# Optimization experiments

Hardware: AMD Instinct MI355X
Metric: run time of the kernel (lower is better)

Reference implementation:

```python
import jax, jax.numpy as jnp
import numpy as np

N_NODES = 1048576
N_EDGES = 4 * N_NODES

def _mlp(h, w1, b1, w2, b2):
    return jax.nn.relu(h @ w1 + b1) @ w2 + b2

def setup_inputs() -> dict:
    key = jax.random.key(0)
    ks = jax.random.split(key, 12)
    def glorot(k, shape):
        fan_in, fan_out = shape
        lim = np.sqrt(6.0 / (fan_in + fan_out)).astype(np.float32)
        return jax.random.uniform(k, shape, jnp.float32, -lim, lim)
    x = jax.random.normal(ks[0], (N_NODES, 3), jnp.float32)
    edge_index = jax.random.randint(ks[1], (2, N_EDGES), 0, N_NODES, jnp.int64 if jax.config.jax_enable_x64 else jnp.int32)
    edge_attr = jax.random.normal(ks[2], (N_EDGES, 1), jnp.float32)
    u = jax.random.normal(ks[3], (1, 3), jnp.float32)
    batch = jnp.zeros((N_NODES,), jnp.int32)
    return {
        'x': x, 'edge_index': edge_index, 'edge_attr': edge_attr, 'u': u, 'batch': batch,
        'w1a': glorot(ks[4], (4, 20)), 'b1a': jnp.zeros((20,), jnp.float32),
        'w1b': glorot(ks[5], (20, 3)), 'b1b': jnp.zeros((3,), jnp.float32),
        'w2a': glorot(ks[6], (6, 20)), 'b2a': jnp.zeros((20,), jnp.float32),
        'w2b': glorot(ks[7], (20, 3)), 'b2b': jnp.zeros((3,), jnp.float32),
    }

def reference(x, edge_index, edge_attr, u, batch, w1a, b1a, w1b, b1b, w2a, b2a, w2b, b2b):
    row, col = edge_index[0], edge_index[1]
    n = x.shape[0]
    # gather source node feats, concat edge attr -> [E,4]
    h = jnp.concatenate([x[row], edge_attr], axis=1)
    h = _mlp(h, w1a, b1a, w1b, b1b)                    # [E,3]
    # scatter-mean over destination nodes
    s = jax.ops.segment_sum(h, col, num_segments=n)    # [N,3]
    cnt = jax.ops.segment_sum(jnp.ones((h.shape[0],), h.dtype), col, num_segments=n)
    agg = s / jnp.maximum(cnt, 1.0)[:, None]
    out = _mlp(jnp.concatenate([x, agg], axis=1), w2a, b2a, w2b, b2b)  # [N,3]
    fac = jnp.sqrt(jnp.sum(out ** 2, axis=1, keepdims=True))
    return out / fac
```

## Files before the change

kernel.cpp:

```cpp
#include <hip/hip_runtime.h>


#define SEG  4096
#define P1T  256
#define P1I  (SEG / P1T)
#define BKSH 12
#define BKN  4096
#define NBK  256
#define PFXW 257
#define P2T  1024
#define P2W  (P2T / 64)

union HCvt { _Float16 h; unsigned short u; };

__device__ __forceinline__ float h2f(unsigned short u) {
    HCvt c; c.u = u; return (float)c.h;
}

__device__ __forceinline__ unsigned long long mlp1_pack(
    float in0, float in1, float in2, float in3,
    const float* sw1a, const float* sb1a, const float* sw1b, const float* sb1b)
{
    float h1[20];
#pragma unroll
    for (int j = 0; j < 20; ++j) {
        float v = sb1a[j];
        v = fmaf(in0, sw1a[0 * 20 + j], v);
        v = fmaf(in1, sw1a[1 * 20 + j], v);
        v = fmaf(in2, sw1a[2 * 20 + j], v);
        v = fmaf(in3, sw1a[3 * 20 + j], v);
        h1[j] = v > 0.f ? v : 0.f;
    }
    float o0 = sb1b[0], o1 = sb1b[1], o2 = sb1b[2];
#pragma unroll
    for (int j = 0; j < 20; ++j) {
        o0 = fmaf(h1[j], sw1b[j * 3 + 0], o0);
        o1 = fmaf(h1[j], sw1b[j * 3 + 1], o1);
        o2 = fmaf(h1[j], sw1b[j * 3 + 2], o2);
    }
    o0 = fminf(fmaxf(o0, -8.0f), 8.0f - 2.0f / 2048.0f);
    o1 = fminf(fmaxf(o1, -8.0f), 8.0f - 2.0f / 2048.0f);
    o2 = fminf(fmaxf(o2, -8.0f), 8.0f - 2.0f / 1024.0f);
    const unsigned int q0 = (unsigned int)__float2int_rn((o0 + 8.0f) * 2048.0f);
    const unsigned int q1 = (unsigned int)__float2int_rn((o1 + 8.0f) * 2048.0f);
    const unsigned int q2 = (unsigned int)__float2int_rn((o2 + 8.0f) * 1024.0f);
    return 1ULL | ((unsigned long long)q0 << 5)
                | ((unsigned long long)q1 << 25)
                | ((unsigned long long)q2 << 45);
}

__global__ __launch_bounds__(256) void pack_x_kernel(
    const float* __restrict__ x, ushort4* __restrict__ xp, int N)
{
    const int n = blockIdx.x * 256 + threadIdx.x;
    if (n >= N) return;
    HCvt c0, c1, c2;
    c0.h = (_Float16)x[n * 3 + 0];
    c1.h = (_Float16)x[n * 3 + 1];
    c2.h = (_Float16)x[n * 3 + 2];
    ushort4 r; r.x = c0.u; r.y = c1.u; r.z = c2.u; r.w = 0;
    xp[n] = r;
}

__global__ __launch_bounds__(P1T) void p1_kernel(
    const ushort4* __restrict__ xp,
    const int*   __restrict__ edge_index,
    const float* __restrict__ edge_attr,
    const float* __restrict__ w1a, const float* __restrict__ b1a,
    const float* __restrict__ w1b, const float* __restrict__ b1b,
    unsigned short* __restrict__ pfx_t,
    unsigned short* __restrict__ cols16,
    unsigned long long* __restrict__ vals,
    int E)
{
    __shared__ float sw1a[80], sb1a[20], sw1b[60], sb1b[3];
    __shared__ unsigned int hist[NBK];
    __shared__ unsigned int sc[NBK];
    __shared__ unsigned int pfx[PFXW];
    __shared__ unsigned short scols[SEG];
    __shared__ __align__(16) unsigned long long svals[SEG];
    const int t = threadIdx.x;
    if (t < 80) sw1a[t] = w1a[t];
    if (t < 20) sb1a[t] = b1a[t];
    if (t < 60) sw1b[t] = w1b[t];
    if (t < 3)  sb1b[t] = b1b[t];
    hist[t] = 0;
    __syncthreads();

    const int s = blockIdx.x;
    const int base = s * SEG;

    unsigned int col8[P1I];
#pragma unroll
    for (int i = 0; i < P1I; ++i) {
        const int e = base + i * P1T + t;
        if (e < E) {
            const unsigned int c = (unsigned int)edge_index[E + e];
            col8[i] = c;
            atomicAdd(&hist[c >> BKSH], 1u);
        } else {
            col8[i] = 0xFFFFFFFFu;
        }
    }
    __syncthreads();

    sc[t] = hist[t];
    __syncthreads();
#pragma unroll
    for (int off = 1; off < NBK; off <<= 1) {
        const unsigned int u = (t >= off) ? sc[t - off] : 0u;
        __syncthreads();
        sc[t] += u;
        __syncthreads();
    }
    pfx[t + 1] = sc[t];
    if (t == 0) pfx[0] = 0;
    hist[t] = 0;
    __syncthreads();

    pfx_t[s * PFXW + t] = (unsigned short)pfx[t];
    if (t == 0) pfx_t[s * PFXW + NBK] = (unsigned short)pfx[NBK];

#pragma unroll
    for (int i = 0; i < P1I; ++i) {
        const unsigned int c = col8[i];
        if (c == 0xFFFFFFFFu) continue;
        const int e = base + i * P1T + t;
        const int row = edge_index[e];
        const float in3 = edge_attr[e];
        const ushort4 px = xp[row];
        const float in0 = h2f(px.x);
        const float in1 = h2f(px.y);
        const float in2 = h2f(px.z);
        const unsigned long long val =
            mlp1_pack(in0, in1, in2, in3, sw1a, sb1a, sw1b, sb1b);
        const unsigned int bkt = c >> BKSH;
        const unsigned int r = atomicAdd(&hist[bkt], 1u);
        const unsigned int idx = pfx[bkt] + r;
        scols[idx] = (unsigned short)(c & (BKN - 1));
        svals[idx] = val;
    }
    __syncthreads();

    unsigned int* gc = (unsigned int*)(cols16 + (size_t)base);
    const unsigned int* scu = (const unsigned int*)scols;
#pragma unroll
    for (int k = t; k < SEG / 2; k += P1T) gc[k] = scu[k];
    unsigned long long* gv = vals + (size_t)base;
#pragma unroll
    for (int k = t; k < SEG; k += P1T) gv[k] = svals[k];
}

__global__ __launch_bounds__(P2T) void p2_kernel(
    const float* __restrict__ x,
    const unsigned short* __restrict__ pfx_t,
    const unsigned short* __restrict__ cols16,
    const unsigned long long* __restrict__ vals,
    const float* __restrict__ w2a, const float* __restrict__ b2a,
    const float* __restrict__ w2b, const float* __restrict__ b2b,
    float* __restrict__ out,
    int N, int nsegs)
{
    __shared__ float sw2a[120], sb2a[20], sw2b[60], sb2b[3];
    __shared__ unsigned long long acc[BKN];
    const int t = threadIdx.x;
    if (t < 120) sw2a[t] = w2a[t];
    if (t < 20)  sb2a[t] = b2a[t];
    if (t < 60)  sw2b[t] = w2b[t];
    if (t < 3)   sb2b[t] = b2b[t];
#pragma unroll
    for (int k = 0; k < BKN / P2T; ++k) acc[k * P2T + t] = 0ULL;
    __syncthreads();

    const int b = blockIdx.x;
    const int wave = t >> 6;
    const int lane = t & 63;

    for (int s = wave; s < nsegs; s += P2W) {
        const unsigned int pa = pfx_t[s * PFXW + b];
        const unsigned int pb = pfx_t[s * PFXW + b + 1];
        const size_t base = (size_t)s * SEG;
        for (unsigned int i = pa + lane; i < pb; i += 64) {
            const unsigned int c = cols16[base + i];
            const unsigned long long v = vals[base + i];
            atomicAdd(&acc[c], v);
        }
    }
    __syncthreads();

    const int node0 = b * BKN;
#pragma unroll
    for (int k = 0; k < BKN / P2T; ++k) {
        const int n = node0 + k * P2T + t;
        if (n >= N) continue;
        const unsigned long long q = acc[k * P2T + t];

        const float cnt = (float)(unsigned int)(q & 31ULL);
        const float f0 = (float)(unsigned int)((q >> 5)  & 0xFFFFFULL);
        const float f1 = (float)(unsigned int)((q >> 25) & 0xFFFFFULL);
        const float f2 = (float)(unsigned int)(q >> 45);
        const float s0 = f0 * (1.0f / 2048.0f) - 8.0f * cnt;
        const float s1 = f1 * (1.0f / 2048.0f) - 8.0f * cnt;
        const float s2 = f2 * (1.0f / 1024.0f) - 8.0f * cnt;
        const float invc = 1.0f / fmaxf(cnt, 1.0f);

        const float in0 = x[n * 3 + 0];
        const float in1 = x[n * 3 + 1];
        const float in2 = x[n * 3 + 2];
        const float in3 = s0 * invc;
        const float in4 = s1 * invc;
        const float in5 = s2 * invc;

        float h1[20];
#pragma unroll
        for (int j = 0; j < 20; ++j) {
            float v = sb2a[j];
            v = fmaf(in0, sw2a[0 * 20 + j], v);
            v = fmaf(in1, sw2a[1 * 20 + j], v);
            v = fmaf(in2, sw2a[2 * 20 + j], v);
            v = fmaf(in3, sw2a[3 * 20 + j], v);
            v = fmaf(in4, sw2a[4 * 20 + j], v);
            v = fmaf(in5, sw2a[5 * 20 + j], v);
            h1[j] = v > 0.f ? v : 0.f;
        }
        float o0 = sb2b[0], o1 = sb2b[1], o2 = sb2b[2];
#pragma unroll
        for (int j = 0; j < 20; ++j) {
            o0 = fmaf(h1[j], sw2b[j * 3 + 0], o0);
            o1 = fmaf(h1[j], sw2b[j * 3 + 1], o1);
            o2 = fmaf(h1[j], sw2b[j * 3 + 2], o2);
        }
        const float inv = 1.0f / sqrtf(o0 * o0 + o1 * o1 + o2 * o2);
        out[n * 3 + 0] = o0 * inv;
        out[n * 3 + 1] = o1 * inv;
        out[n * 3 + 2] = o2 * inv;
    }
}

__global__ __launch_bounds__(256) void edge_kernel_fb(
    const float* __restrict__ x, const int* __restrict__ edge_index,
    const float* __restrict__ edge_attr,
    const float* __restrict__ w1a, const float* __restrict__ b1a,
    const float* __restrict__ w1b, const float* __restrict__ b1b,
    unsigned long long* __restrict__ acc, int E)
{
    __shared__ float sw1a[80], sb1a[20], sw1b[60], sb1b[3];
    const int t = threadIdx.x;
    if (t < 80) sw1a[t] = w1a[t];
    if (t < 20) sb1a[t] = b1a[t];
    if (t < 60) sw1b[t] = w1b[t];
    if (t < 3)  sb1b[t] = b1b[t];
    __syncthreads();
    const int e = blockIdx.x * 256 + t;
    if (e >= E) return;
    const int row = edge_index[e];
    const int col = edge_index[E + e];
    const unsigned long long val = mlp1_pack(
        x[row * 3 + 0], x[row * 3 + 1], x[row * 3 + 2], edge_attr[e],
        sw1a, sb1a, sw1b, sb1b);
    atomicAdd(acc + col, val);
}

__global__ __launch_bounds__(256) void node_kernel_fb(
    const float* __restrict__ x, const unsigned long long* __restrict__ acc,
    const float* __restrict__ w2a, const float* __restrict__ b2a,
    const float* __restrict__ w2b, const float* __restrict__ b2b,
    float* __restrict__ out, int N)
{
    __shared__ float sw2a[120], sb2a[20], sw2b[60], sb2b[3];
    const int t = threadIdx.x;
    if (t < 120) sw2a[t] = w2a[t];
    if (t < 20)  sb2a[t] = b2a[t];
    if (t < 60)  sw2b[t] = w2b[t];
    if (t < 3)   sb2b[t] = b2b[t];
    __syncthreads();
    const int n = blockIdx.x * 256 + t;
    if (n >= N) return;
    const unsigned long long q = acc[n];
    const float cnt = (float)(unsigned int)(q & 31ULL);
    const float f0 = (float)(unsigned int)((q >> 5)  & 0xFFFFFULL);
    const float f1 = (float)(unsigned int)((q >> 25) & 0xFFFFFULL);
    const float f2 = (float)(unsigned int)(q >> 45);
    const float s0 = f0 * (1.0f / 2048.0f) - 8.0f * cnt;
    const float s1 = f1 * (1.0f / 2048.0f) - 8.0f * cnt;
    const float s2 = f2 * (1.0f / 1024.0f) - 8.0f * cnt;
    const float invc = 1.0f / fmaxf(cnt, 1.0f);
    const float in0 = x[n * 3 + 0], in1 = x[n * 3 + 1], in2 = x[n * 3 + 2];
    const float in3 = s0 * invc, in4 = s1 * invc, in5 = s2 * invc;
    float h1[20];
#pragma unroll
    for (int j = 0; j < 20; ++j) {
        float v = sb2a[j];
        v = fmaf(in0, sw2a[0 * 20 + j], v);
        v = fmaf(in1, sw2a[1 * 20 + j], v);
        v = fmaf(in2, sw2a[2 * 20 + j], v);
        v = fmaf(in3, sw2a[3 * 20 + j], v);
        v = fmaf(in4, sw2a[4 * 20 + j], v);
        v = fmaf(in5, sw2a[5 * 20 + j], v);
        h1[j] = v > 0.f ? v : 0.f;
    }
    float o0 = sb2b[0], o1 = sb2b[1], o2 = sb2b[2];
#pragma unroll
    for (int j = 0; j < 20; ++j) {
        o0 = fmaf(h1[j], sw2b[j * 3 + 0], o0);
        o1 = fmaf(h1[j], sw2b[j * 3 + 1], o1);
        o2 = fmaf(h1[j], sw2b[j * 3 + 2], o2);
    }
    const float inv = 1.0f / sqrtf(o0 * o0 + o1 * o1 + o2 * o2);
    out[n * 3 + 0] = o0 * inv;
    out[n * 3 + 1] = o1 * inv;
    out[n * 3 + 2] = o2 * inv;
}

extern "C" void kernel_launch(void* const* d_in, const int* in_sizes, int n_in,
                              void* d_out, int out_size, void* d_ws, size_t ws_size,
                              hipStream_t stream) {
    const float* x          = (const float*)d_in[0];
    const int*   edge_index = (const int*)  d_in[1];
    const float* edge_attr  = (const float*)d_in[2];
    const float* w1a = (const float*)d_in[5];
    const float* b1a = (const float*)d_in[6];
    const float* w1b = (const float*)d_in[7];
    const float* b1b = (const float*)d_in[8];
    const float* w2a = (const float*)d_in[9];
    const float* b2a = (const float*)d_in[10];
    const float* w2b = (const float*)d_in[11];
    const float* b2b = (const float*)d_in[12];

    const int N = in_sizes[0] / 3;
    const int E = in_sizes[2];

    const int nbuckets = (N + BKN - 1) / BKN;
    const int nsegs = (E + SEG - 1) / SEG;

    const size_t xp_bytes   = (size_t)N * sizeof(ushort4);
    const size_t pfx_off    = (xp_bytes + 255) & ~(size_t)255;
    const size_t pfx_bytes  = (size_t)nsegs * PFXW * sizeof(unsigned short);
    const size_t cols_off   = (pfx_off + pfx_bytes + 255) & ~(size_t)255;
    const size_t cols_bytes = (size_t)nsegs * SEG * sizeof(unsigned short);
    const size_t vals_off   = (cols_off + cols_bytes + 255) & ~(size_t)255;
    const size_t need       = vals_off + (size_t)nsegs * SEG * sizeof(unsigned long long);

    const bool fast = (nbuckets <= NBK) && (ws_size >= need);

    if (fast) {
        ushort4* xp = (ushort4*)d_ws;
        unsigned short* pfx_t  = (unsigned short*)((char*)d_ws + pfx_off);
        unsigned short* cols16 = (unsigned short*)((char*)d_ws + cols_off);
        unsigned long long* vals = (unsigned long long*)((char*)d_ws + vals_off);

        pack_x_kernel<<<(N + 255) / 256, 256, 0, stream>>>(x, xp, N);

        p1_kernel<<<nsegs, P1T, 0, stream>>>(
            xp, edge_index, edge_attr, w1a, b1a, w1b, b1b,
            pfx_t, cols16, vals, E);

        p2_kernel<<<nbuckets, P2T, 0, stream>>>(
            x, pfx_t, cols16, vals, w2a, b2a, w2b, b2b,
            (float*)d_out, N, nsegs);
    } else {
        unsigned long long* acc = (unsigned long long*)d_ws;
        hipMemsetAsync(acc, 0, (size_t)N * sizeof(unsigned long long), stream);
        edge_kernel_fb<<<(E + 255) / 256, 256, 0, stream>>>(
            x, edge_index, edge_attr, w1a, b1a, w1b, b1b, acc, E);
        node_kernel_fb<<<(N + 255) / 256, 256, 0, stream>>>(
            x, acc, w2a, b2a, w2b, b2b, (float*)d_out, N);
    }
}
```

Measured before the change: 238.9 us.

## Split bucket aggregation into two half-blocks and separate node MLP kernel

The per-bucket scatter-add phase now runs as two blocks per bucket, each covering half of the segments and writing a partial accumulator to global memory. A new elementwise kernel sums the two partials and runs the node MLP and normalisation. The prefix table is stored transposed so each bucket reads a contiguous row, and the edge kernel block grows to 512 threads. The goal is more blocks in flight than 256 buckets give, at the cost of an extra launch and a round trip of the partial sums through global memory.

Measured after the change: 283.4 us. 18.6% more time.

```diff
diff --git a/kernel.cpp b/kernel.cpp
--- a/kernel.cpp
+++ b/kernel.cpp
@@ -2,14 +2,13 @@
 
 
 #define SEG  4096
-#define P1T  256
+#define P1T  512
 #define P1I  (SEG / P1T)
 #define BKSH 12
 #define BKN  4096
 #define NBK  256
 #define PFXW 257
-#define P2T  1024
-#define P2W  (P2T / 64)
+#define P2AT 512
 
 union HCvt { _Float16 h; unsigned short u; };
 
@@ -49,6 +48,51 @@
                 | ((unsigned long long)q2 << 45);
 }
 
+__device__ __forceinline__ void mlp2_store(
+    unsigned long long q, const float* __restrict__ x, float* __restrict__ out,
+    int n, const float* sw2a, const float* sb2a, const float* sw2b, const float* sb2b)
+{
+    const float cnt = (float)(unsigned int)(q & 31ULL);
+    const float f0 = (float)(unsigned int)((q >> 5)  & 0xFFFFFULL);
+    const float f1 = (float)(unsigned int)((q >> 25) & 0xFFFFFULL);
+    const float f2 = (float)(unsigned int)(q >> 45);
+    const float s0 = f0 * (1.0f / 2048.0f) - 8.0f * cnt;
+    const float s1 = f1 * (1.0f / 2048.0f) - 8.0f * cnt;
+    const float s2 = f2 * (1.0f / 1024.0f) - 8.0f * cnt;
+    const float invc = 1.0f / fmaxf(cnt, 1.0f);
+
+    const float in0 = x[n * 3 + 0];
+    const float in1 = x[n * 3 + 1];
+    const float in2 = x[n * 3 + 2];
+    const float in3 = s0 * invc;
+    const float in4 = s1 * invc;
+    const float in5 = s2 * invc;
+
+    float h1[20];
+#pragma unroll
+    for (int j = 0; j < 20; ++j) {
+        float v = sb2a[j];
+        v = fmaf(in0, sw2a[0 * 20 + j], v);
+        v = fmaf(in1, sw2a[1 * 20 + j], v);
+        v = fmaf(in2, sw2a[2 * 20 + j], v);
+        v = fmaf(in3, sw2a[3 * 20 + j], v);
+        v = fmaf(in4, sw2a[4 * 20 + j], v);
+        v = fmaf(in5, sw2a[5 * 20 + j], v);
+        h1[j] = v > 0.f ? v : 0.f;
+    }
+    float o0 = sb2b[0], o1 = sb2b[1], o2 = sb2b[2];
+#pragma unroll
+    for (int j = 0; j < 20; ++j) {
+        o0 = fmaf(h1[j], sw2b[j * 3 + 0], o0);
+        o1 = fmaf(h1[j], sw2b[j * 3 + 1], o1);
+        o2 = fmaf(h1[j], sw2b[j * 3 + 2], o2);
+    }
+    const float inv = 1.0f / sqrtf(o0 * o0 + o1 * o1 + o2 * o2);
+    out[n * 3 + 0] = o0 * inv;
+    out[n * 3 + 1] = o1 * inv;
+    out[n * 3 + 2] = o2 * inv;
+}
+
 __global__ __launch_bounds__(256) void pack_x_kernel(
     const float* __restrict__ x, ushort4* __restrict__ xp, int N)
 {
@@ -62,16 +106,16 @@
     xp[n] = r;
 }
 
-__global__ __launch_bounds__(P1T) void p1_kernel(
+__global__ __launch_bounds__(P1T, 4) void p1_kernel(
     const ushort4* __restrict__ xp,
     const int*   __restrict__ edge_index,
     const float* __restrict__ edge_attr,
     const float* __restrict__ w1a, const float* __restrict__ b1a,
     const float* __restrict__ w1b, const float* __restrict__ b1b,
-    unsigned short* __restrict__ pfx_t,
+    unsigned short* __restrict__ pfx_tr,
     unsigned short* __restrict__ cols16,
     unsigned long long* __restrict__ vals,
-    int E)
+    int E, int nsegs)
 {
     __shared__ float sw1a[80], sb1a[20], sw1b[60], sb1b[3];
     __shared__ unsigned int hist[NBK];
@@ -84,7 +128,7 @@
     if (t < 20) sb1a[t] = b1a[t];
     if (t < 60) sw1b[t] = w1b[t];
     if (t < 3)  sb1b[t] = b1b[t];
-    hist[t] = 0;
+    if (t < NBK) hist[t] = 0;
     __syncthreads();
 
     const int s = blockIdx.x;
@@ -104,22 +148,22 @@
     }
     __syncthreads();
 
-    sc[t] = hist[t];
+    if (t < NBK) sc[t] = hist[t];
     __syncthreads();
 #pragma unroll
     for (int off = 1; off < NBK; off <<= 1) {
-        const unsigned int u = (t >= off) ? sc[t - off] : 0u;
+        unsigned int u = 0;
+        if (t < NBK && t >= off) u = sc[t - off];
         __syncthreads();
-        sc[t] += u;
+        if (t < NBK) sc[t] += u;
         __syncthreads();
     }
-    pfx[t + 1] = sc[t];
+    if (t < NBK) pfx[t + 1] = sc[t];
     if (t == 0) pfx[0] = 0;
-    hist[t] = 0;
-    __syncthreads();
-
-    pfx_t[s * PFXW + t] = (unsigned short)pfx[t];
-    if (t == 0) pfx_t[s * PFXW + NBK] = (unsigned short)pfx[NBK];
+    if (t < NBK) hist[t] = 0;
+    __syncthreads();
+
+    if (t < PFXW) pfx_tr[(size_t)t * nsegs + s] = (unsigned short)pfx[t];
 
 #pragma unroll
     for (int i = 0; i < P1I; ++i) {
@@ -151,34 +195,29 @@
     for (int k = t; k < SEG; k += P1T) gv[k] = svals[k];
 }
 
-__global__ __launch_bounds__(P2T) void p2_kernel(
-    const float* __restrict__ x,
-    const unsigned short* __restrict__ pfx_t,
+__global__ __launch_bounds__(P2AT) void p2a_kernel(
+    const unsigned short* __restrict__ pfx_tr,
     const unsigned short* __restrict__ cols16,
     const unsigned long long* __restrict__ vals,
-    const float* __restrict__ w2a, const float* __restrict__ b2a,
-    const float* __restrict__ w2b, const float* __restrict__ b2b,
-    float* __restrict__ out,
-    int N, int nsegs)
-{
-    __shared__ float sw2a[120], sb2a[20], sw2b[60], sb2b[3];
+    unsigned long long* __restrict__ partial,
+    int nsegs)
+{
     __shared__ unsigned long long acc[BKN];
     const int t = threadIdx.x;
-    if (t < 120) sw2a[t] = w2a[t];
-    if (t < 20)  sb2a[t] = b2a[t];
-    if (t < 60)  sw2b[t] = w2b[t];
-    if (t < 3)   sb2b[t] = b2b[t];
-#pragma unroll
-    for (int k = 0; k < BKN / P2T; ++k) acc[k * P2T + t] = 0ULL;
-    __syncthreads();
-
-    const int b = blockIdx.x;
+#pragma unroll
+    for (int k = t; k < BKN; k += P2AT) acc[k] = 0ULL;
+    __syncthreads();
+
+    const int b = blockIdx.x >> 1;
+    const int h = blockIdx.x & 1;
     const int wave = t >> 6;
     const int lane = t & 63;
-
-    for (int s = wave; s < nsegs; s += P2W) {
-        const unsigned int pa = pfx_t[s * PFXW + b];
-        const unsigned int pb = pfx_t[s * PFXW + b + 1];
+    const unsigned short* rowa = pfx_tr + (size_t)b * nsegs;
+    const unsigned short* rowb = pfx_tr + (size_t)(b + 1) * nsegs;
+
+    for (int s = h + 2 * wave; s < nsegs; s += 2 * (P2AT / 64)) {
+        const unsigned int pa = rowa[s];
+        const unsigned int pb = rowb[s];
         const size_t base = (size_t)s * SEG;
         for (unsigned int i = pa + lane; i < pb; i += 64) {
             const unsigned int c = cols16[base + i];
@@ -188,53 +227,36 @@
     }
     __syncthreads();
 
-    const int node0 = b * BKN;
-#pragma unroll
-    for (int k = 0; k < BKN / P2T; ++k) {
-        const int n = node0 + k * P2T + t;
-        if (n >= N) continue;
-        const unsigned long long q = acc[k * P2T + t];
-
-        const float cnt = (float)(unsigned int)(q & 31ULL);
-        const float f0 = (float)(unsigned int)((q >> 5)  & 0xFFFFFULL);
-        const float f1 = (float)(unsigned int)((q >> 25) & 0xFFFFFULL);
-        const float f2 = (float)(unsigned int)(q >> 45);
-        const float s0 = f0 * (1.0f / 2048.0f) - 8.0f * cnt;
-        const float s1 = f1 * (1.0f / 2048.0f) - 8.0f * cnt;
-        const float s2 = f2 * (1.0f / 1024.0f) - 8.0f * cnt;
-        const float invc = 1.0f / fmaxf(cnt, 1.0f);
-
-        const float in0 = x[n * 3 + 0];
-        const float in1 = x[n * 3 + 1];
-        const float in2 = x[n * 3 + 2];
-        const float in3 = s0 * invc;
-        const float in4 = s1 * invc;
-        const float in5 = s2 * invc;
-
-        float h1[20];
-#pragma unroll
-        for (int j = 0; j < 20; ++j) {
-            float v = sb2a[j];
-            v = fmaf(in0, sw2a[0 * 20 + j], v);
-            v = fmaf(in1, sw2a[1 * 20 + j], v);
-            v = fmaf(in2, sw2a[2 * 20 + j], v);
-            v = fmaf(in3, sw2a[3 * 20 + j], v);
-            v = fmaf(in4, sw2a[4 * 20 + j], v);
-            v = fmaf(in5, sw2a[5 * 20 + j], v);
-            h1[j] = v > 0.f ? v : 0.f;
-        }
-        float o0 = sb2b[0], o1 = sb2b[1], o2 = sb2b[2];
-#pragma unroll
-        for (int j = 0; j < 20; ++j) {
-            o0 = fmaf(h1[j], sw2b[j * 3 + 0], o0);
-            o1 = fmaf(h1[j], sw2b[j * 3 + 1], o1);
-            o2 = fmaf(h1[j], sw2b[j * 3 + 2], o2);
-        }
-        const float inv = 1.0f / sqrtf(o0 * o0 + o1 * o1 + o2 * o2);
-        out[n * 3 + 0] = o0 * inv;
-        out[n * 3 + 1] = o1 * inv;
-        out[n * 3 + 2] = o2 * inv;
-    }
+    unsigned long long* dst = partial + (size_t)blockIdx.x * BKN;
+#pragma unroll
+    for (int k = t; k < BKN; k += P2AT) dst[k] = acc[k];
+}
+
+__global__ __launch_bounds__(256) void p2b_kernel(
+    const float* __restrict__ x,
+    const unsigned long long* __restrict__ partial,
+    const float* __restrict__ w2a, const float* __restrict__ b2a,
+    const float* __restrict__ w2b, const float* __restrict__ b2b,
+    float* __restrict__ out, int N)
+{
+    __shared__ float sw2a[120], sb2a[20], sw2b[60], sb2b[3];
+    const int t = threadIdx.x;
+    if (t < 120) sw2a[t] = w2a[t];
+    if (t < 20)  sb2a[t] = b2a[t];
+    if (t < 60)  sw2b[t] = w2b[t];
+    if (t < 3)   sb2b[t] = b2b[t];
+    __syncthreads();
+
+    const int n = blockIdx.x * 256 + t;
+    if (n >= N) return;
+
+    const int bkt = n >> BKSH;
+    const int idx = n & (BKN - 1);
+    const unsigned long long q =
+        partial[(size_t)(2 * bkt) * BKN + idx] +
+        partial[(size_t)(2 * bkt + 1) * BKN + idx];
+
+    mlp2_store(q, x, out, n, sw2a, sb2a, sw2b, sb2b);
 }
 
 __global__ __launch_bounds__(256) void edge_kernel_fb(
@@ -276,40 +298,7 @@
     __syncthreads();
     const int n = blockIdx.x * 256 + t;
     if (n >= N) return;
-    const unsigned long long q = acc[n];
-    const float cnt = (float)(unsigned int)(q & 31ULL);
-    const float f0 = (float)(unsigned int)((q >> 5)  & 0xFFFFFULL);
-    const float f1 = (float)(unsigned int)((q >> 25) & 0xFFFFFULL);
-    const float f2 = (float)(unsigned int)(q >> 45);
-    const float s0 = f0 * (1.0f / 2048.0f) - 8.0f * cnt;
-    const float s1 = f1 * (1.0f / 2048.0f) - 8.0f * cnt;
-    const float s2 = f2 * (1.0f / 1024.0f) - 8.0f * cnt;
-    const float invc = 1.0f / fmaxf(cnt, 1.0f);
-    const float in0 = x[n * 3 + 0], in1 = x[n * 3 + 1], in2 = x[n * 3 + 2];
-    const float in3 = s0 * invc, in4 = s1 * invc, in5 = s2 * invc;
-    float h1[20];
-#pragma unroll
-    for (int j = 0; j < 20; ++j) {
-        float v = sb2a[j];
-        v = fmaf(in0, sw2a[0 * 20 + j], v);
-        v = fmaf(in1, sw2a[1 * 20 + j], v);
-        v = fmaf(in2, sw2a[2 * 20 + j], v);
-        v = fmaf(in3, sw2a[3 * 20 + j], v);
-        v = fmaf(in4, sw2a[4 * 20 + j], v);
-        v = fmaf(in5, sw2a[5 * 20 + j], v);
-        h1[j] = v > 0.f ? v : 0.f;
-    }
-    float o0 = sb2b[0], o1 = sb2b[1], o2 = sb2b[2];
-#pragma unroll
-    for (int j = 0; j < 20; ++j) {
-        o0 = fmaf(h1[j], sw2b[j * 3 + 0], o0);
-        o1 = fmaf(h1[j], sw2b[j * 3 + 1], o1);
-        o2 = fmaf(h1[j], sw2b[j * 3 + 2], o2);
-    }
-    const float inv = 1.0f / sqrtf(o0 * o0 + o1 * o1 + o2 * o2);
-    out[n * 3 + 0] = o0 * inv;
-    out[n * 3 + 1] = o1 * inv;
-    out[n * 3 + 2] = o2 * inv;
+    mlp2_store(acc[n], x, out, n, sw2a, sb2a, sw2b, sb2b);
 }
 
 extern "C" void kernel_launch(void* const* d_in, const int* in_sizes, int n_in,
@@ -333,9 +322,11 @@
     const int nbuckets = (N + BKN - 1) / BKN;
     const int nsegs = (E + SEG - 1) / SEG;
 
+    const size_t part_bytes = (size_t)nbuckets * 2 * BKN * sizeof(unsigned long long);
     const size_t xp_bytes   = (size_t)N * sizeof(ushort4);
-    const size_t pfx_off    = (xp_bytes + 255) & ~(size_t)255;
-    const size_t pfx_bytes  = (size_t)nsegs * PFXW * sizeof(unsigned short);
+    const size_t region0    = part_bytes > xp_bytes ? part_bytes : xp_bytes;
+    const size_t pfx_off    = (region0 + 255) & ~(size_t)255;
+    const size_t pfx_bytes  = (size_t)PFXW * nsegs * sizeof(unsigned short);
     const size_t cols_off   = (pfx_off + pfx_bytes + 255) & ~(size_t)255;
     const size_t cols_bytes = (size_t)nsegs * SEG * sizeof(unsigned short);
     const size_t vals_off   = (cols_off + cols_bytes + 255) & ~(size_t)255;
@@ -345,7 +336,8 @@
 
     if (fast) {
         ushort4* xp = (ushort4*)d_ws;
-        unsigned short* pfx_t  = (unsigned short*)((char*)d_ws + pfx_off);
+        unsigned long long* partial = (unsigned long long*)d_ws;
+        unsigned short* pfx_tr = (unsigned short*)((char*)d_ws + pfx_off);
         unsigned short* cols16 = (unsigned short*)((char*)d_ws + cols_off);
         unsigned long long* vals = (unsigned long long*)((char*)d_ws + vals_off);
 
@@ -353,11 +345,13 @@
 
         p1_kernel<<<nsegs, P1T, 0, stream>>>(
             xp, edge_index, edge_attr, w1a, b1a, w1b, b1b,
-            pfx_t, cols16, vals, E);
-
-        p2_kernel<<<nbuckets, P2T, 0, stream>>>(
-            x, pfx_t, cols16, vals, w2a, b2a, w2b, b2b,
-            (float*)d_out, N, nsegs);
+            pfx_tr, cols16, vals, E, nsegs);
+
+        p2a_kernel<<<nbuckets * 2, P2AT, 0, stream>>>(
+            pfx_tr, cols16, vals, partial, nsegs);
+
+        p2b_kernel<<<(N + 255) / 256, 256, 0, stream>>>(
+            x, partial, w2a, b2a, w2b, b2b, (float*)d_out, N);
     } else {
         unsigned long long* acc = (unsigned long long*)d_ws;
         hipMemsetAsync(acc, 0, (size_t)N * sizeof(unsigned long long), stream);
```

## Pack column index into edge record and transpose bucket prefix table

Applied to the files above, without the earlier changes.

The 12-bit local column index is folded into each 64-bit edge record, so the separate 16-bit column array is dropped, along with its shared-memory staging and global write and read. p2 unpacks the record into the accumulator format before its atomic add. The per-segment prefix table is transposed so each bucket block reads a contiguous row of offsets. This cuts global traffic and the shared-memory footprint in p1, at the cost of a little extra bit manipulation per edge in p2.

After: 240.4 us. No clear change (+0.6%).

```diff
diff --git a/kernel.cpp b/kernel.cpp
--- a/kernel.cpp
+++ b/kernel.cpp
@@ -9,7 +9,6 @@
 #define NBK  256
 #define PFXW 257
 #define P2T  1024
-#define P2W  (P2T / 64)
 
 union HCvt { _Float16 h; unsigned short u; };
 
@@ -17,9 +16,10 @@
     HCvt c; c.u = u; return (float)c.h;
 }
 
-__device__ __forceinline__ unsigned long long mlp1_pack(
+__device__ __forceinline__ void mlp1_eval(
     float in0, float in1, float in2, float in3,
-    const float* sw1a, const float* sb1a, const float* sw1b, const float* sb1b)
+    const float* sw1a, const float* sb1a, const float* sw1b, const float* sb1b,
+    float& o0, float& o1, float& o2)
 {
     float h1[20];
 #pragma unroll
@@ -31,7 +31,7 @@
         v = fmaf(in3, sw1a[3 * 20 + j], v);
         h1[j] = v > 0.f ? v : 0.f;
     }
-    float o0 = sb1b[0], o1 = sb1b[1], o2 = sb1b[2];
+    o0 = sb1b[0]; o1 = sb1b[1]; o2 = sb1b[2];
 #pragma unroll
     for (int j = 0; j < 20; ++j) {
         o0 = fmaf(h1[j], sw1b[j * 3 + 0], o0);
@@ -41,12 +41,68 @@
     o0 = fminf(fmaxf(o0, -8.0f), 8.0f - 2.0f / 2048.0f);
     o1 = fminf(fmaxf(o1, -8.0f), 8.0f - 2.0f / 2048.0f);
     o2 = fminf(fmaxf(o2, -8.0f), 8.0f - 2.0f / 1024.0f);
-    const unsigned int q0 = (unsigned int)__float2int_rn((o0 + 8.0f) * 2048.0f);
-    const unsigned int q1 = (unsigned int)__float2int_rn((o1 + 8.0f) * 2048.0f);
-    const unsigned int q2 = (unsigned int)__float2int_rn((o2 + 8.0f) * 1024.0f);
-    return 1ULL | ((unsigned long long)q0 << 5)
-                | ((unsigned long long)q1 << 25)
-                | ((unsigned long long)q2 << 45);
+}
+
+__device__ __forceinline__ unsigned long long rec_pack(
+    unsigned int col_lo, float o0, float o1, float o2)
+{
+    const unsigned long long q0 = (unsigned int)__float2int_rn((o0 + 8.0f) * 2048.0f);
+    const unsigned long long q1 = (unsigned int)__float2int_rn((o1 + 8.0f) * 2048.0f);
+    const unsigned long long q2 = (unsigned int)__float2int_rn((o2 + 8.0f) * 1024.0f);
+    return (unsigned long long)col_lo | (q0 << 12) | (q1 << 27) | (q2 << 42);
+}
+
+__device__ __forceinline__ unsigned long long acc_pack(float o0, float o1, float o2)
+{
+    const unsigned long long q0 = (unsigned int)__float2int_rn((o0 + 8.0f) * 2048.0f);
+    const unsigned long long q1 = (unsigned int)__float2int_rn((o1 + 8.0f) * 2048.0f);
+    const unsigned long long q2 = (unsigned int)__float2int_rn((o2 + 8.0f) * 1024.0f);
+    return 1ULL | (q0 << 5) | (q1 << 25) | (q2 << 45);
+}
+
+__device__ __forceinline__ void mlp2_store(
+    unsigned long long q, const float* __restrict__ x, float* __restrict__ out,
+    int n, const float* sw2a, const float* sb2a, const float* sw2b, const float* sb2b)
+{
+    const float cnt = (float)(unsigned int)(q & 31ULL);
+    const float f0 = (float)(unsigned int)((q >> 5)  & 0xFFFFFULL);
+    const float f1 = (float)(unsigned int)((q >> 25) & 0xFFFFFULL);
+    const float f2 = (float)(unsigned int)(q >> 45);
+    const float s0 = f0 * (1.0f / 2048.0f) - 8.0f * cnt;
+    const float s1 = f1 * (1.0f / 2048.0f) - 8.0f * cnt;
+    const float s2 = f2 * (1.0f / 1024.0f) - 8.0f * cnt;
+    const float invc = 1.0f / fmaxf(cnt, 1.0f);
+
+    const float in0 = x[n * 3 + 0];
+    const float in1 = x[n * 3 + 1];
+    const float in2 = x[n * 3 + 2];
+    const float in3 = s0 * invc;
+    const float in4 = s1 * invc;
+    const float in5 = s2 * invc;
+
+    float h1[20];
+#pragma unroll
+    for (int j = 0; j < 20; ++j) {
+        float v = sb2a[j];
+        v = fmaf(in0, sw2a[0 * 20 + j], v);
+        v = fmaf(in1, sw2a[1 * 20 + j], v);
+        v = fmaf(in2, sw2a[2 * 20 + j], v);
+        v = fmaf(in3, sw2a[3 * 20 + j], v);
+        v = fmaf(in4, sw2a[4 * 20 + j], v);
+        v = fmaf(in5, sw2a[5 * 20 + j], v);
+        h1[j] = v > 0.f ? v : 0.f;
+    }
+    float o0 = sb2b[0], o1 = sb2b[1], o2 = sb2b[2];
+#pragma unroll
+    for (int j = 0; j < 20; ++j) {
+        o0 = fmaf(h1[j], sw2b[j * 3 + 0], o0);
+        o1 = fmaf(h1[j], sw2b[j * 3 + 1], o1);
+        o2 = fmaf(h1[j], sw2b[j * 3 + 2], o2);
+    }
+    const float inv = 1.0f / sqrtf(o0 * o0 + o1 * o1 + o2 * o2);
+    out[n * 3 + 0] = o0 * inv;
+    out[n * 3 + 1] = o1 * inv;
+    out[n * 3 + 2] = o2 * inv;
 }
 
 __global__ __launch_bounds__(256) void pack_x_kernel(
@@ -68,16 +124,14 @@
     const float* __restrict__ edge_attr,
     const float* __restrict__ w1a, const float* __restrict__ b1a,
     const float* __restrict__ w1b, const float* __restrict__ b1b,
-    unsigned short* __restrict__ pfx_t,
-    unsigned short* __restrict__ cols16,
+    unsigned short* __restrict__ pfx_tr,
     unsigned long long* __restrict__ vals,
-    int E)
+    int E, int nsegs)
 {
     __shared__ float sw1a[80], sb1a[20], sw1b[60], sb1b[3];
     __shared__ unsigned int hist[NBK];
     __shared__ unsigned int sc[NBK];
     __shared__ unsigned int pfx[PFXW];
-    __shared__ unsigned short scols[SEG];
     __shared__ __align__(16) unsigned long long svals[SEG];
     const int t = threadIdx.x;
     if (t < 80) sw1a[t] = w1a[t];
@@ -118,8 +172,8 @@
     hist[t] = 0;
     __syncthreads();
 
-    pfx_t[s * PFXW + t] = (unsigned short)pfx[t];
-    if (t == 0) pfx_t[s * PFXW + NBK] = (unsigned short)pfx[NBK];
+    pfx_tr[(size_t)t * nsegs + s] = (unsigned short)pfx[t];
+    if (t == 0) pfx_tr[(size_t)NBK * nsegs + s] = (unsigned short)pfx[NBK];
 
 #pragma unroll
     for (int i = 0; i < P1I; ++i) {
@@ -129,23 +183,16 @@
         const int row = edge_index[e];
         const float in3 = edge_attr[e];
         const ushort4 px = xp[row];
-        const float in0 = h2f(px.x);
-        const float in1 = h2f(px.y);
-        const float in2 = h2f(px.z);
-        const unsigned long long val =
-            mlp1_pack(in0, in1, in2, in3, sw1a, sb1a, sw1b, sb1b);
+        float o0, o1, o2;
+        mlp1_eval(h2f(px.x), h2f(px.y), h2f(px.z), in3,
+                  sw1a, sb1a, sw1b, sb1b, o0, o1, o2);
         const unsigned int bkt = c >> BKSH;
         const unsigned int r = atomicAdd(&hist[bkt], 1u);
         const unsigned int idx = pfx[bkt] + r;
-        scols[idx] = (unsigned short)(c & (BKN - 1));
-        svals[idx] = val;
-    }
-    __syncthreads();
-
-    unsigned int* gc = (unsigned int*)(cols16 + (size_t)base);
-    const unsigned int* scu = (const unsigned int*)scols;
-#pragma unroll
-    for (int k = t; k < SEG / 2; k += P1T) gc[k] = scu[k];
+        svals[idx] = rec_pack(c & (BKN - 1), o0, o1, o2);
+    }
+    __syncthreads();
+
     unsigned long long* gv = vals + (size_t)base;
 #pragma unroll
     for (int k = t; k < SEG; k += P1T) gv[k] = svals[k];
@@ -153,8 +200,7 @@
 
 __global__ __launch_bounds__(P2T) void p2_kernel(
     const float* __restrict__ x,
-    const unsigned short* __restrict__ pfx_t,
-    const unsigned short* __restrict__ cols16,
+    const unsigned short* __restrict__ pfx_tr,
     const unsigned long long* __restrict__ vals,
     const float* __restrict__ w2a, const float* __restrict__ b2a,
     const float* __restrict__ w2b, const float* __restrict__ b2b,
@@ -175,15 +221,22 @@
     const int b = blockIdx.x;
     const int wave = t >> 6;
     const int lane = t & 63;
-
-    for (int s = wave; s < nsegs; s += P2W) {
-        const unsigned int pa = pfx_t[s * PFXW + b];
-        const unsigned int pb = pfx_t[s * PFXW + b + 1];
+    const unsigned short* rowa = pfx_tr + (size_t)b * nsegs;
+    const unsigned short* rowb = pfx_tr + (size_t)(b + 1) * nsegs;
+
+    for (int s = wave; s < nsegs; s += P2T / 64) {
+        const unsigned int pa = rowa[s];
+        const unsigned int pb = rowb[s];
         const size_t base = (size_t)s * SEG;
         for (unsigned int i = pa + lane; i < pb; i += 64) {
-            const unsigned int c = cols16[base + i];
-            const unsigned long long v = vals[base + i];
-            atomicAdd(&acc[c], v);
+            const unsigned long long rec = vals[base + i];
+            const unsigned int c = (unsigned int)(rec & 0xFFFULL);
+            const unsigned long long q0 = (rec >> 12) & 0x7FFFULL;
+            const unsigned long long q1 = (rec >> 27) & 0x7FFFULL;
+            const unsigned long long q2 = (rec >> 42) & 0x3FFFULL;
+            const unsigned long long add =
+                1ULL | (q0 << 5) | (q1 << 25) | (q2 << 45);
+            atomicAdd(&acc[c], add);
         }
     }
     __syncthreads();
@@ -193,47 +246,7 @@
     for (int k = 0; k < BKN / P2T; ++k) {
         const int n = node0 + k * P2T + t;
         if (n >= N) continue;
-        const unsigned long long q = acc[k * P2T + t];
-
-        const float cnt = (float)(unsigned int)(q & 31ULL);
-        const float f0 = (float)(unsigned int)((q >> 5)  & 0xFFFFFULL);
-        const float f1 = (float)(unsigned int)((q >> 25) & 0xFFFFFULL);
-        const float f2 = (float)(unsigned int)(q >> 45);
-        const float s0 = f0 * (1.0f / 2048.0f) - 8.0f * cnt;
-        const float s1 = f1 * (1.0f / 2048.0f) - 8.0f * cnt;
-        const float s2 = f2 * (1.0f / 1024.0f) - 8.0f * cnt;
-        const float invc = 1.0f / fmaxf(cnt, 1.0f);
-
-        const float in0 = x[n * 3 + 0];
-        const float in1 = x[n * 3 + 1];
-        const float in2 = x[n * 3 + 2];
-        const float in3 = s0 * invc;
-        const float in4 = s1 * invc;
-        const float in5 = s2 * invc;
-
-        float h1[20];
-#pragma unroll
-        for (int j = 0; j < 20; ++j) {
-            float v = sb2a[j];
-            v = fmaf(in0, sw2a[0 * 20 + j], v);
-            v = fmaf(in1, sw2a[1 * 20 + j], v);
-            v = fmaf(in2, sw2a[2 * 20 + j], v);
-            v = fmaf(in3, sw2a[3 * 20 + j], v);
-            v = fmaf(in4, sw2a[4 * 20 + j], v);
-            v = fmaf(in5, sw2a[5 * 20 + j], v);
-            h1[j] = v > 0.f ? v : 0.f;
-        }
-        float o0 = sb2b[0], o1 = sb2b[1], o2 = sb2b[2];
-#pragma unroll
-        for (int j = 0; j < 20; ++j) {
-            o0 = fmaf(h1[j], sw2b[j * 3 + 0], o0);
-            o1 = fmaf(h1[j], sw2b[j * 3 + 1], o1);
-            o2 = fmaf(h1[j], sw2b[j * 3 + 2], o2);
-        }
-        const float inv = 1.0f / sqrtf(o0 * o0 + o1 * o1 + o2 * o2);
-        out[n * 3 + 0] = o0 * inv;
-        out[n * 3 + 1] = o1 * inv;
-        out[n * 3 + 2] = o2 * inv;
+        mlp2_store(acc[k * P2T + t], x, out, n, sw2a, sb2a, sw2b, sb2b);
     }
 }
 
@@ -255,10 +268,10 @@
     if (e >= E) return;
     const int row = edge_index[e];
     const int col = edge_index[E + e];
-    const unsigned long long val = mlp1_pack(
-        x[row * 3 + 0], x[row * 3 + 1], x[row * 3 + 2], edge_attr[e],
-        sw1a, sb1a, sw1b, sb1b);
-    atomicAdd(acc + col, val);
+    float o0, o1, o2;
+    mlp1_eval(x[row * 3 + 0], x[row * 3 + 1], x[row * 3 + 2], edge_attr[e],
+              sw1a, sb1a, sw1b, sb1b, o0, o1, o2);
+    atomicAdd(acc + col, acc_pack(o0, o1, o2));
 }
 
 __global__ __launch_bounds__(256) void node_kernel_fb(
@@ -276,40 +289,7 @@
     __syncthreads();
     const int n = blockIdx.x * 256 + t;
     if (n >= N) return;
-    const unsigned long long q = acc[n];
-    const float cnt = (float)(unsigned int)(q & 31ULL);
-    const float f0 = (float)(unsigned int)((q >> 5)  & 0xFFFFFULL);
-    const float f1 = (float)(unsigned int)((q >> 25) & 0xFFFFFULL);
-    const float f2 = (float)(unsigned int)(q >> 45);
-    const float s0 = f0 * (1.0f / 2048.0f) - 8.0f * cnt;
-    const float s1 = f1 * (1.0f / 2048.0f) - 8.0f * cnt;
-    const float s2 = f2 * (1.0f / 1024.0f) - 8.0f * cnt;
-    const float invc = 1.0f / fmaxf(cnt, 1.0f);
-    const float in0 = x[n * 3 + 0], in1 = x[n * 3 + 1], in2 = x[n * 3 + 2];
-    const float in3 = s0 * invc, in4 = s1 * invc, in5 = s2 * invc;
-    float h1[20];
-#pragma unroll
-    for (int j = 0; j < 20; ++j) {
-        float v = sb2a[j];
-        v = fmaf(in0, sw2a[0 * 20 + j], v);
-        v = fmaf(in1, sw2a[1 * 20 + j], v);
-        v = fmaf(in2, sw2a[2 * 20 + j], v);
-        v = fmaf(in3, sw2a[3 * 20 + j], v);
-        v = fmaf(in4, sw2a[4 * 20 + j], v);
-        v = fmaf(in5, sw2a[5 * 20 + j], v);
-        h1[j] = v > 0.f ? v : 0.f;
-    }
-    float o0 = sb2b[0], o1 = sb2b[1], o2 = sb2b[2];
-#pragma unroll
-    for (int j = 0; j < 20; ++j) {
-        o0 = fmaf(h1[j], sw2b[j * 3 + 0], o0);
-        o1 = fmaf(h1[j], sw2b[j * 3 + 1], o1);
-        o2 = fmaf(h1[j], sw2b[j * 3 + 2], o2);
-    }
-    const float inv = 1.0f / sqrtf(o0 * o0 + o1 * o1 + o2 * o2);
-    out[n * 3 + 0] = o0 * inv;
-    out[n * 3 + 1] = o1 * inv;
-    out[n * 3 + 2] = o2 * inv;
+    mlp2_store(acc[n], x, out, n, sw2a, sb2a, sw2b, sb2b);
 }
 
 extern "C" void kernel_launch(void* const* d_in, const int* in_sizes, int n_in,
@@ -333,31 +313,27 @@
     const int nbuckets = (N + BKN - 1) / BKN;
     const int nsegs = (E + SEG - 1) / SEG;
 
-    const size_t xp_bytes   = (size_t)N * sizeof(ushort4);
-    const size_t pfx_off    = (xp_bytes + 255) & ~(size_t)255;
-    const size_t pfx_bytes  = (size_t)nsegs * PFXW * sizeof(unsigned short);
-    const size_t cols_off   = (pfx_off + pfx_bytes + 255) & ~(size_t)255;
-    const size_t cols_bytes = (size_t)nsegs * SEG * sizeof(unsigned short);
-    const size_t vals_off   = (cols_off + cols_bytes + 255) & ~(size_t)255;
-    const size_t need       = vals_off + (size_t)nsegs * SEG * sizeof(unsigned long long);
+    const size_t xp_bytes  = (size_t)N * sizeof(ushort4);
+    const size_t pfx_off   = (xp_bytes + 255) & ~(size_t)255;
+    const size_t pfx_bytes = (size_t)PFXW * nsegs * sizeof(unsigned short);
+    const size_t vals_off  = (pfx_off + pfx_bytes + 255) & ~(size_t)255;
+    const size_t need      = vals_off + (size_t)nsegs * SEG * sizeof(unsigned long long);
 
     const bool fast = (nbuckets <= NBK) && (ws_size >= need);
 
     if (fast) {
         ushort4* xp = (ushort4*)d_ws;
-        unsigned short* pfx_t  = (unsigned short*)((char*)d_ws + pfx_off);
-        unsigned short* cols16 = (unsigned short*)((char*)d_ws + cols_off);
+        unsigned short* pfx_tr = (unsigned short*)((char*)d_ws + pfx_off);
         unsigned long long* vals = (unsigned long long*)((char*)d_ws + vals_off);
 
         pack_x_kernel<<<(N + 255) / 256, 256, 0, stream>>>(x, xp, N);
 
         p1_kernel<<<nsegs, P1T, 0, stream>>>(
             xp, edge_index, edge_attr, w1a, b1a, w1b, b1b,
-            pfx_t, cols16, vals, E);
+            pfx_tr, vals, E, nsegs);
 
         p2_kernel<<<nbuckets, P2T, 0, stream>>>(
-            x, pfx_t, cols16, vals, w2a, b2a, w2b, b2b,
-            (float*)d_out, N, nsegs);
+            x, pfx_tr, vals, w2a, b2a, w2b, b2b, (float*)d_out, N, nsegs);
     } else {
         unsigned long long* acc = (unsigned long long*)d_ws;
         hipMemsetAsync(acc, 0, (size_t)N * sizeof(unsigned long long), stream);
```
